# Performance work log

Measured on AMD Instinct MI355X. Metric: run time of the kernel, lower is better.

The kernel has to match this reference:

```python
import jax, jax.numpy as jnp
import numpy as np

T, B, D_IN, D_H, D_MID, D_OUT = 16, 16384, 64, 256, 64, 4


def setup_inputs() -> dict:
    key = jax.random.key(0)
    ks = jax.random.split(key, 12)
    s = 0.05
    return {
        "x": jax.random.normal(ks[0], (T, B, D_IN), dtype=jnp.float32),
        "hc1": jnp.zeros((B, D_H), dtype=jnp.float32),
        "W_i2h": jax.random.normal(ks[1], (D_H, D_IN), dtype=jnp.float32) * s,
        "b_i2h": jax.random.normal(ks[2], (D_H,), dtype=jnp.float32) * s,
        "W_h2h": jax.random.normal(ks[3], (D_H, D_H), dtype=jnp.float32) * s,
        "b_h2h": jax.random.normal(ks[4], (D_H,), dtype=jnp.float32) * s,
        "W_h2o": jax.random.normal(ks[5], (D_MID, D_H), dtype=jnp.float32) * s,
        "b_h2o": jax.random.normal(ks[6], (D_MID,), dtype=jnp.float32) * s,
        "W_fc": jax.random.normal(ks[7], (D_OUT, D_MID), dtype=jnp.float32) * s,
        "b_fc": jax.random.normal(ks[8], (D_OUT,), dtype=jnp.float32) * s,
    }


def reference(x, hc1, W_i2h, b_i2h, W_h2h, b_h2h, W_h2o, b_h2o, W_fc, b_fc):
    # 16-step vanilla RNN: h = tanh(i2h(x_t) + h2h(h)); out = fc(tanh(h2o(h)))
    def step(h, xt):
        h_new = jnp.tanh(xt @ W_i2h.T + b_i2h + h @ W_h2h.T + b_h2h)  # [B, 256]
        out = jnp.tanh(h_new @ W_h2o.T + b_h2o) @ W_fc.T + b_fc       # [B, 4]
        return h_new, out

    h_final, output_seq = jax.lax.scan(step, hc1, x)
    return output_seq, h_final
```

## Files before the change

kernel.cpp:

```cpp
#include <hip/hip_runtime.h>


typedef _Float16 half8 __attribute__((ext_vector_type(8)));
typedef _Float16 half4 __attribute__((ext_vector_type(4)));
typedef float floatx4 __attribute__((ext_vector_type(4)));

#define T_STEPS  16
#define BATCH    16384
#define BLK_ROWS 32
#define HS       264
#define XS       72
#define MS       72

#define WS_WI 0
#define WS_WH 16384
#define WS_WO 81920
#define WS_WF 98304
#define WS_TOT 98560

__global__ void prep_kernel(const float* __restrict__ Wi, const float* __restrict__ Wh,
                            const float* __restrict__ Wo, const float* __restrict__ Wf,
                            _Float16* __restrict__ ws) {
    int i = blockIdx.x * 256 + threadIdx.x;
    if (i >= WS_TOT) return;
    float v;
    if (i < WS_WH)      v = Wi[i];
    else if (i < WS_WO) v = Wh[i - WS_WH];
    else if (i < WS_WF) v = Wo[i - WS_WO];
    else                v = Wf[i - WS_WF];
    ws[i] = (_Float16)v;
}

__device__ inline float fast_tanh(float x) {
    float t = __builtin_amdgcn_exp2f(x * 2.8853900817779268f);
    return 1.0f - 2.0f * __builtin_amdgcn_rcpf(t + 1.0f);
}

__device__ inline half8 cvt8pair(float4 a, float4 b) {
    half8 h;
    h[0] = (_Float16)a.x; h[1] = (_Float16)a.y; h[2] = (_Float16)a.z; h[3] = (_Float16)a.w;
    h[4] = (_Float16)b.x; h[5] = (_Float16)b.y; h[6] = (_Float16)b.z; h[7] = (_Float16)b.w;
    return h;
}

#define MFMA(a, b, c) __builtin_amdgcn_mfma_f32_16x16x32_f16((a), (b), (c), 0, 0, 0)

__global__ __launch_bounds__(512, 2) void rnn_kernel(
    const float* __restrict__ x,    const float* __restrict__ hc1,
    const _Float16* __restrict__ wf16,
    const float* __restrict__ bi,   const float* __restrict__ bh,
    const float* __restrict__ bo,   const float* __restrict__ bfc,
    float* __restrict__ out)
{
    __shared__ _Float16 h_lds[2][BLK_ROWS * HS];
    __shared__ _Float16 xf[2][BLK_ROWS * XS];
    __shared__ _Float16 midb[2][BLK_ROWS * MS];
    __shared__ _Float16 wfc_lds[256];

    const int tid  = threadIdx.x;
    const int w    = tid >> 6;
    const int lane = tid & 63;
    const int l16  = lane & 15;
    const int quad = lane >> 4;
    const int b0   = blockIdx.x * BLK_ROWS;

    if (tid < 256) wfc_lds[tid] = wf16[WS_WF + tid];

    float bpre[2];
    #pragma unroll
    for (int nt = 0; nt < 2; ++nt) {
        int c = w * 32 + nt * 16 + l16;
        bpre[nt] = bi[c] + bh[c];
    }
    const int midc  = (w >> 1) * 16 + l16;
    const int midmt = w & 1;
    float bo_r  = bo[midc];
    float bfc_r = (tid < 128) ? bfc[tid & 3] : 0.0f;

    half8 wcat[10][2];
    #pragma unroll
    for (int ks = 0; ks < 10; ++ks) {
        #pragma unroll
        for (int nt = 0; nt < 2; ++nt) {
            int j = w * 32 + nt * 16 + l16;
            wcat[ks][nt] = (ks < 2)
                ? *(const half8*)(wf16 + WS_WI + (size_t)j * 64  + ks * 32 + quad * 8)
                : *(const half8*)(wf16 + WS_WH + (size_t)j * 256 + (ks - 2) * 32 + quad * 8);
        }
    }

    {
        int rr = tid >> 4, c0 = (tid & 15) * 16;
        const float4* s = (const float4*)&hc1[(size_t)(b0 + rr) * 256 + c0];
        float4 a = s[0], b = s[1], c = s[2], d = s[3];
        *(half8*)&h_lds[0][rr * HS + c0]     = cvt8pair(a, b);
        *(half8*)&h_lds[0][rr * HS + c0 + 8] = cvt8pair(c, d);
    }
    {
        int rr = tid >> 4, c0 = (tid & 15) * 4;
        float4 v = *(const float4*)&x[(size_t)(b0 + rr) * 64 + c0];
        half4 h; h[0] = (_Float16)v.x; h[1] = (_Float16)v.y; h[2] = (_Float16)v.z; h[3] = (_Float16)v.w;
        *(half4*)&xf[0][rr * XS + c0] = h;
    }

    __syncthreads();

    for (int r = 0; r < T_STEPS + 2; ++r) {
        const int cur = r & 1, nxt = cur ^ 1;

        if (r < T_STEPS) {
            float4 xv;
            const int xrow = tid >> 4, xc0 = (tid & 15) * 4;
            if (r <= T_STEPS - 2)
                xv = *(const float4*)&x[((size_t)(r + 1) * BATCH + b0 + xrow) * 64 + xc0];

            #pragma unroll
            for (int mt = 0; mt < 2; ++mt) {
                floatx4 acc0 = {0.f, 0.f, 0.f, 0.f};
                floatx4 acc1 = {0.f, 0.f, 0.f, 0.f};
                const int arow = mt * 16 + l16;
                #pragma unroll
                for (int ks = 0; ks < 8; ++ks) {
                    half8 af = *(const half8*)&h_lds[cur][arow * HS + ks * 32 + quad * 8];
                    acc0 = MFMA(af, wcat[2 + ks][0], acc0);
                    acc1 = MFMA(af, wcat[2 + ks][1], acc1);
                }
                #pragma unroll
                for (int ks = 0; ks < 2; ++ks) {
                    half8 af = *(const half8*)&xf[cur][arow * XS + ks * 32 + quad * 8];
                    acc0 = MFMA(af, wcat[ks][0], acc0);
                    acc1 = MFMA(af, wcat[ks][1], acc1);
                }
                #pragma unroll
                for (int rr2 = 0; rr2 < 4; ++rr2) {
                    int row = mt * 16 + quad * 4 + rr2;
                    h_lds[nxt][row * HS + w * 32 + l16]      = (_Float16)fast_tanh(acc0[rr2] + bpre[0]);
                    h_lds[nxt][row * HS + w * 32 + 16 + l16] = (_Float16)fast_tanh(acc1[rr2] + bpre[1]);
                }
            }
            if (r <= T_STEPS - 2) {
                half4 h; h[0] = (_Float16)xv.x; h[1] = (_Float16)xv.y; h[2] = (_Float16)xv.z; h[3] = (_Float16)xv.w;
                *(half4*)&xf[nxt][xrow * XS + xc0] = h;
            }
        }

        if (r >= 1 && r <= T_STEPS) {
            floatx4 acc2 = {0.f, 0.f, 0.f, 0.f};
            #pragma unroll
            for (int hv = 0; hv < 2; ++hv) {
                half8 wo4[4];
                #pragma unroll
                for (int i = 0; i < 4; ++i)
                    wo4[i] = *(const half8*)(wf16 + WS_WO + (size_t)midc * 256 + (hv * 4 + i) * 32 + quad * 8);
                #pragma unroll
                for (int i = 0; i < 4; ++i) {
                    half8 af = *(const half8*)&h_lds[cur][(midmt * 16 + l16) * HS + (hv * 4 + i) * 32 + quad * 8];
                    acc2 = MFMA(af, wo4[i], acc2);
                }
            }
            #pragma unroll
            for (int rr2 = 0; rr2 < 4; ++rr2) {
                int row = midmt * 16 + quad * 4 + rr2;
                midb[cur][row * MS + midc] = (_Float16)fast_tanh(acc2[rr2] + bo_r);
            }
        }

        if (tid < 128 && r >= 2) {
            int row = tid >> 2, oc = tid & 3;
            float s = bfc_r;
            #pragma unroll
            for (int k8 = 0; k8 < 64; k8 += 8) {
                half8 mv = *(const half8*)&midb[nxt][row * MS + k8];
                half8 wv = *(const half8*)&wfc_lds[oc * 64 + k8];
                #pragma unroll
                for (int j = 0; j < 8; ++j)
                    s += (float)mv[j] * (float)wv[j];
            }
            out[((size_t)(r - 2) * BATCH + b0 + row) * 4 + oc] = s;
        }

        __syncthreads();
    }

    {
        int rr = tid >> 4, c0 = (tid & 15) * 16;
        half8 p0 = *(const half8*)&h_lds[0][rr * HS + c0];
        half8 p1 = *(const half8*)&h_lds[0][rr * HS + c0 + 8];
        float4* dst = (float4*)&out[(size_t)T_STEPS * BATCH * 4 + (size_t)(b0 + rr) * 256 + c0];
        float4 v;
        v.x = (float)p0[0]; v.y = (float)p0[1]; v.z = (float)p0[2]; v.w = (float)p0[3]; dst[0] = v;
        v.x = (float)p0[4]; v.y = (float)p0[5]; v.z = (float)p0[6]; v.w = (float)p0[7]; dst[1] = v;
        v.x = (float)p1[0]; v.y = (float)p1[1]; v.z = (float)p1[2]; v.w = (float)p1[3]; dst[2] = v;
        v.x = (float)p1[4]; v.y = (float)p1[5]; v.z = (float)p1[6]; v.w = (float)p1[7]; dst[3] = v;
    }
}

extern "C" void kernel_launch(void* const* d_in, const int* in_sizes, int n_in,
                              void* d_out, int out_size, void* d_ws, size_t ws_size,
                              hipStream_t stream) {
    const float* x   = (const float*)d_in[0];
    const float* hc1 = (const float*)d_in[1];
    const float* Wi  = (const float*)d_in[2];
    const float* bi  = (const float*)d_in[3];
    const float* Wh  = (const float*)d_in[4];
    const float* bh  = (const float*)d_in[5];
    const float* Wo  = (const float*)d_in[6];
    const float* bo  = (const float*)d_in[7];
    const float* Wf  = (const float*)d_in[8];
    const float* bf  = (const float*)d_in[9];
    _Float16* ws = (_Float16*)d_ws;

    prep_kernel<<<(WS_TOT + 255) / 256, 256, 0, stream>>>(Wi, Wh, Wo, Wf, ws);
    rnn_kernel<<<BATCH / BLK_ROWS, 512, 0, stream>>>(
        x, hc1, ws, bi, bh, bo, bf, (float*)d_out);
}
```

Measured before the change: 227.9 us.

## Halve block to 4 waves, fuse h2o MFMA into recurrence, MFMA the fc layer

```diff
diff --git a/kernel.cpp b/kernel.cpp
--- a/kernel.cpp
+++ b/kernel.cpp
@@ -2,7 +2,6 @@
 
 
 typedef _Float16 half8 __attribute__((ext_vector_type(8)));
-typedef _Float16 half4 __attribute__((ext_vector_type(4)));
 typedef float floatx4 __attribute__((ext_vector_type(4)));
 
 #define T_STEPS  16
@@ -16,7 +15,7 @@
 #define WS_WH 16384
 #define WS_WO 81920
 #define WS_WF 98304
-#define WS_TOT 98560
+#define WS_TOT 99328
 
 __global__ void prep_kernel(const float* __restrict__ Wi, const float* __restrict__ Wh,
                             const float* __restrict__ Wo, const float* __restrict__ Wf,
@@ -24,10 +23,11 @@
     int i = blockIdx.x * 256 + threadIdx.x;
     if (i >= WS_TOT) return;
     float v;
-    if (i < WS_WH)      v = Wi[i];
-    else if (i < WS_WO) v = Wh[i - WS_WH];
-    else if (i < WS_WF) v = Wo[i - WS_WO];
-    else                v = Wf[i - WS_WF];
+    if (i < WS_WH)           v = Wi[i];
+    else if (i < WS_WO)      v = Wh[i - WS_WH];
+    else if (i < WS_WF)      v = Wo[i - WS_WO];
+    else if (i < WS_WF + 256) v = Wf[i - WS_WF];
+    else                     v = 0.0f;
     ws[i] = (_Float16)v;
 }
 
@@ -45,7 +45,7 @@
 
 #define MFMA(a, b, c) __builtin_amdgcn_mfma_f32_16x16x32_f16((a), (b), (c), 0, 0, 0)
 
-__global__ __launch_bounds__(512, 2) void rnn_kernel(
+__global__ __launch_bounds__(256, 2) void rnn_kernel(
     const float* __restrict__ x,    const float* __restrict__ hc1,
     const _Float16* __restrict__ wf16,
     const float* __restrict__ bi,   const float* __restrict__ bh,
@@ -55,7 +55,6 @@
     __shared__ _Float16 h_lds[2][BLK_ROWS * HS];
     __shared__ _Float16 xf[2][BLK_ROWS * XS];
     __shared__ _Float16 midb[2][BLK_ROWS * MS];
-    __shared__ _Float16 wfc_lds[256];
 
     const int tid  = threadIdx.x;
     const int w    = tid >> 6;
@@ -64,25 +63,22 @@
     const int quad = lane >> 4;
     const int b0   = blockIdx.x * BLK_ROWS;
 
-    if (tid < 256) wfc_lds[tid] = wf16[WS_WF + tid];
-
-    float bpre[2];
+    float bpre[4];
     #pragma unroll
-    for (int nt = 0; nt < 2; ++nt) {
-        int c = w * 32 + nt * 16 + l16;
+    for (int nt = 0; nt < 4; ++nt) {
+        int c = w * 64 + nt * 16 + l16;
         bpre[nt] = bi[c] + bh[c];
     }
-    const int midc  = (w >> 1) * 16 + l16;
-    const int midmt = w & 1;
+    const int midc = w * 16 + l16;
     float bo_r  = bo[midc];
-    float bfc_r = (tid < 128) ? bfc[tid & 3] : 0.0f;
-
-    half8 wcat[10][2];
+    float bfc_r = bfc[l16 & 3];
+
+    half8 wcat[10][4];
     #pragma unroll
     for (int ks = 0; ks < 10; ++ks) {
         #pragma unroll
-        for (int nt = 0; nt < 2; ++nt) {
-            int j = w * 32 + nt * 16 + l16;
+        for (int nt = 0; nt < 4; ++nt) {
+            int j = w * 64 + nt * 16 + l16;
             wcat[ks][nt] = (ks < 2)
                 ? *(const half8*)(wf16 + WS_WI + (size_t)j * 64  + ks * 32 + quad * 8)
                 : *(const half8*)(wf16 + WS_WH + (size_t)j * 256 + (ks - 2) * 32 + quad * 8);
@@ -90,17 +86,19 @@
     }
 
     {
-        int rr = tid >> 4, c0 = (tid & 15) * 16;
+        int rr = tid >> 3, c0 = (tid & 7) * 32;
         const float4* s = (const float4*)&hc1[(size_t)(b0 + rr) * 256 + c0];
         float4 a = s[0], b = s[1], c = s[2], d = s[3];
-        *(half8*)&h_lds[0][rr * HS + c0]     = cvt8pair(a, b);
-        *(half8*)&h_lds[0][rr * HS + c0 + 8] = cvt8pair(c, d);
+        float4 e = s[4], f = s[5], g = s[6], hh = s[7];
+        *(half8*)&h_lds[0][rr * HS + c0]      = cvt8pair(a, b);
+        *(half8*)&h_lds[0][rr * HS + c0 + 8]  = cvt8pair(c, d);
+        *(half8*)&h_lds[0][rr * HS + c0 + 16] = cvt8pair(e, f);
+        *(half8*)&h_lds[0][rr * HS + c0 + 24] = cvt8pair(g, hh);
     }
     {
-        int rr = tid >> 4, c0 = (tid & 15) * 4;
-        float4 v = *(const float4*)&x[(size_t)(b0 + rr) * 64 + c0];
-        half4 h; h[0] = (_Float16)v.x; h[1] = (_Float16)v.y; h[2] = (_Float16)v.z; h[3] = (_Float16)v.w;
-        *(half4*)&xf[0][rr * XS + c0] = h;
+        int rr = tid >> 3, c0 = (tid & 7) * 8;
+        const float4* s = (const float4*)&x[(size_t)(b0 + rr) * 64 + c0];
+        *(half8*)&xf[0][rr * XS + c0] = cvt8pair(s[0], s[1]);
     }
 
     __syncthreads();
@@ -109,89 +107,122 @@
         const int cur = r & 1, nxt = cur ^ 1;
 
         if (r < T_STEPS) {
-            float4 xv;
-            const int xrow = tid >> 4, xc0 = (tid & 15) * 4;
-            if (r <= T_STEPS - 2)
-                xv = *(const float4*)&x[((size_t)(r + 1) * BATCH + b0 + xrow) * 64 + xc0];
+            float4 xa, xb;
+            const int xr = tid >> 3, xc = (tid & 7) * 8;
+            if (r < T_STEPS - 1) {
+                const float* xp = x + ((size_t)(r + 1) * BATCH + b0 + xr) * 64 + xc;
+                xa = ((const float4*)xp)[0];
+                xb = ((const float4*)xp)[1];
+            }
 
             #pragma unroll
             for (int mt = 0; mt < 2; ++mt) {
-                floatx4 acc0 = {0.f, 0.f, 0.f, 0.f};
-                floatx4 acc1 = {0.f, 0.f, 0.f, 0.f};
+                floatx4 a0 = {0.f,0.f,0.f,0.f}, a1 = {0.f,0.f,0.f,0.f};
+                floatx4 a2 = {0.f,0.f,0.f,0.f}, a3 = {0.f,0.f,0.f,0.f};
+                floatx4 am = {0.f,0.f,0.f,0.f};
                 const int arow = mt * 16 + l16;
                 #pragma unroll
-                for (int ks = 0; ks < 8; ++ks) {
-                    half8 af = *(const half8*)&h_lds[cur][arow * HS + ks * 32 + quad * 8];
-                    acc0 = MFMA(af, wcat[2 + ks][0], acc0);
-                    acc1 = MFMA(af, wcat[2 + ks][1], acc1);
+                for (int hv = 0; hv < 2; ++hv) {
+                    half8 wo4[4];
+                    #pragma unroll
+                    for (int i = 0; i < 4; ++i)
+                        wo4[i] = *(const half8*)(wf16 + WS_WO + (size_t)midc * 256 + (hv * 4 + i) * 32 + quad * 8);
+                    #pragma unroll
+                    for (int i = 0; i < 4; ++i) {
+                        const int ks = hv * 4 + i;
+                        half8 af = *(const half8*)&h_lds[cur][arow * HS + ks * 32 + quad * 8];
+                        a0 = MFMA(af, wcat[2 + ks][0], a0);
+                        a1 = MFMA(af, wcat[2 + ks][1], a1);
+                        a2 = MFMA(af, wcat[2 + ks][2], a2);
+                        a3 = MFMA(af, wcat[2 + ks][3], a3);
+                        am = MFMA(af, wo4[i], am);
+                    }
                 }
                 #pragma unroll
                 for (int ks = 0; ks < 2; ++ks) {
                     half8 af = *(const half8*)&xf[cur][arow * XS + ks * 32 + quad * 8];
-                    acc0 = MFMA(af, wcat[ks][0], acc0);
-                    acc1 = MFMA(af, wcat[ks][1], acc1);
-                }
-                #pragma unroll
-                for (int rr2 = 0; rr2 < 4; ++rr2) {
-                    int row = mt * 16 + quad * 4 + rr2;
-                    h_lds[nxt][row * HS + w * 32 + l16]      = (_Float16)fast_tanh(acc0[rr2] + bpre[0]);
-                    h_lds[nxt][row * HS + w * 32 + 16 + l16] = (_Float16)fast_tanh(acc1[rr2] + bpre[1]);
-                }
-            }
-            if (r <= T_STEPS - 2) {
-                half4 h; h[0] = (_Float16)xv.x; h[1] = (_Float16)xv.y; h[2] = (_Float16)xv.z; h[3] = (_Float16)xv.w;
-                *(half4*)&xf[nxt][xrow * XS + xc0] = h;
-            }
-        }
-
-        if (r >= 1 && r <= T_STEPS) {
-            floatx4 acc2 = {0.f, 0.f, 0.f, 0.f};
+                    a0 = MFMA(af, wcat[ks][0], a0);
+                    a1 = MFMA(af, wcat[ks][1], a1);
+                    a2 = MFMA(af, wcat[ks][2], a2);
+                    a3 = MFMA(af, wcat[ks][3], a3);
+                }
+                #pragma unroll
+                for (int rr = 0; rr < 4; ++rr) {
+                    int row = mt * 16 + quad * 4 + rr;
+                    _Float16* hd = &h_lds[nxt][row * HS + w * 64 + l16];
+                    hd[0]  = (_Float16)fast_tanh(a0[rr] + bpre[0]);
+                    hd[16] = (_Float16)fast_tanh(a1[rr] + bpre[1]);
+                    hd[32] = (_Float16)fast_tanh(a2[rr] + bpre[2]);
+                    hd[48] = (_Float16)fast_tanh(a3[rr] + bpre[3]);
+                    if (r >= 1)
+                        midb[cur][row * MS + midc] = (_Float16)fast_tanh(am[rr] + bo_r);
+                }
+            }
+
+            if (r < T_STEPS - 1) {
+                half8 hx = cvt8pair(xa, xb);
+                *(half8*)&xf[nxt][xr * XS + xc] = hx;
+            }
+        } else if (r == T_STEPS) {
             #pragma unroll
-            for (int hv = 0; hv < 2; ++hv) {
-                half8 wo4[4];
-                #pragma unroll
-                for (int i = 0; i < 4; ++i)
-                    wo4[i] = *(const half8*)(wf16 + WS_WO + (size_t)midc * 256 + (hv * 4 + i) * 32 + quad * 8);
-                #pragma unroll
-                for (int i = 0; i < 4; ++i) {
-                    half8 af = *(const half8*)&h_lds[cur][(midmt * 16 + l16) * HS + (hv * 4 + i) * 32 + quad * 8];
-                    acc2 = MFMA(af, wo4[i], acc2);
-                }
-            }
+            for (int mt = 0; mt < 2; ++mt) {
+                floatx4 am = {0.f,0.f,0.f,0.f};
+                const int arow = mt * 16 + l16;
+                #pragma unroll
+                for (int hv = 0; hv < 2; ++hv) {
+                    half8 wo4[4];
+                    #pragma unroll
+                    for (int i = 0; i < 4; ++i)
+                        wo4[i] = *(const half8*)(wf16 + WS_WO + (size_t)midc * 256 + (hv * 4 + i) * 32 + quad * 8);
+                    #pragma unroll
+                    for (int i = 0; i < 4; ++i) {
+                        half8 af = *(const half8*)&h_lds[cur][arow * HS + (hv * 4 + i) * 32 + quad * 8];
+                        am = MFMA(af, wo4[i], am);
+                    }
+                }
+                #pragma unroll
+                for (int rr = 0; rr < 4; ++rr) {
+                    int row = mt * 16 + quad * 4 + rr;
+                    midb[cur][row * MS + midc] = (_Float16)fast_tanh(am[rr] + bo_r);
+                }
+            }
+        }
+
+        if (r >= 2 && w == 3) {
+            half8 wb0 = *(const half8*)(wf16 + WS_WF + (size_t)l16 * 64 + quad * 8);
+            half8 wb1 = *(const half8*)(wf16 + WS_WF + (size_t)l16 * 64 + 32 + quad * 8);
             #pragma unroll
-            for (int rr2 = 0; rr2 < 4; ++rr2) {
-                int row = midmt * 16 + quad * 4 + rr2;
-                midb[cur][row * MS + midc] = (_Float16)fast_tanh(acc2[rr2] + bo_r);
-            }
-        }
-
-        if (tid < 128 && r >= 2) {
-            int row = tid >> 2, oc = tid & 3;
-            float s = bfc_r;
-            #pragma unroll
-            for (int k8 = 0; k8 < 64; k8 += 8) {
-                half8 mv = *(const half8*)&midb[nxt][row * MS + k8];
-                half8 wv = *(const half8*)&wfc_lds[oc * 64 + k8];
-                #pragma unroll
-                for (int j = 0; j < 8; ++j)
-                    s += (float)mv[j] * (float)wv[j];
-            }
-            out[((size_t)(r - 2) * BATCH + b0 + row) * 4 + oc] = s;
+            for (int mt = 0; mt < 2; ++mt) {
+                floatx4 ac = {0.f,0.f,0.f,0.f};
+                half8 af0 = *(const half8*)&midb[nxt][(mt * 16 + l16) * MS + quad * 8];
+                half8 af1 = *(const half8*)&midb[nxt][(mt * 16 + l16) * MS + 32 + quad * 8];
+                ac = MFMA(af0, wb0, ac);
+                ac = MFMA(af1, wb1, ac);
+                if (l16 < 4) {
+                    #pragma unroll
+                    for (int rr = 0; rr < 4; ++rr) {
+                        int row = mt * 16 + quad * 4 + rr;
+                        out[((size_t)(r - 2) * BATCH + b0 + row) * 4 + l16] = ac[rr] + bfc_r;
+                    }
+                }
+            }
         }
 
         __syncthreads();
     }
 
     {
-        int rr = tid >> 4, c0 = (tid & 15) * 16;
-        half8 p0 = *(const half8*)&h_lds[0][rr * HS + c0];
-        half8 p1 = *(const half8*)&h_lds[0][rr * HS + c0 + 8];
+        int rr = tid >> 3, c0 = (tid & 7) * 32;
         float4* dst = (float4*)&out[(size_t)T_STEPS * BATCH * 4 + (size_t)(b0 + rr) * 256 + c0];
-        float4 v;
-        v.x = (float)p0[0]; v.y = (float)p0[1]; v.z = (float)p0[2]; v.w = (float)p0[3]; dst[0] = v;
-        v.x = (float)p0[4]; v.y = (float)p0[5]; v.z = (float)p0[6]; v.w = (float)p0[7]; dst[1] = v;
-        v.x = (float)p1[0]; v.y = (float)p1[1]; v.z = (float)p1[2]; v.w = (float)p1[3]; dst[2] = v;
-        v.x = (float)p1[4]; v.y = (float)p1[5]; v.z = (float)p1[6]; v.w = (float)p1[7]; dst[3] = v;
+        #pragma unroll
+        for (int p = 0; p < 4; ++p) {
+            half8 v = *(const half8*)&h_lds[0][rr * HS + c0 + p * 8];
+            float4 o0, o1;
+            o0.x = (float)v[0]; o0.y = (float)v[1]; o0.z = (float)v[2]; o0.w = (float)v[3];
+            o1.x = (float)v[4]; o1.y = (float)v[5]; o1.z = (float)v[6]; o1.w = (float)v[7];
+            dst[p * 2]     = o0;
+            dst[p * 2 + 1] = o1;
+        }
     }
 }
 
@@ -211,6 +242,6 @@
     _Float16* ws = (_Float16*)d_ws;
 
     prep_kernel<<<(WS_TOT + 255) / 256, 256, 0, stream>>>(Wi, Wh, Wo, Wf, ws);
-    rnn_kernel<<<BATCH / BLK_ROWS, 512, 0, stream>>>(
+    rnn_kernel<<<BATCH / BLK_ROWS, 256, 0, stream>>>(
         x, hc1, ws, bi, bh, bo, bf, (float*)d_out);
 }
```

Result: slower. 349.0 us (+53.2%).
